# Performance work log

Hardware: AMD Instinct MI355X
Metric: run time of the kernel (lower is better)

The kernel has to match this reference:

```python
import math
import jax, jax.numpy as jnp
import numpy as np

B, S, C, H, W = 2, 4, 64, 256, 256
CI = 3 * C + 2      # per-sweep router input channels (Sz,Tz,delta + 2 pos)
CO = CI // 8        # compress_ratio = 8 -> 24
ENC = S * CO        # 96
HID = 64
TEMP = 0.7
ALPHA_ADV, BETA_BAND = 1.0, 0.5
BAND_L, BAND_H = 0.05, 0.2
W_HEUR, W_LEAR = 0.5, 0.5


def group_norm(x, gamma, beta, groups, eps=1e-5):
    b, c, h, w = x.shape
    xg = x.reshape(b, groups, c // groups, h, w)
    mu = xg.mean(axis=(2, 3, 4), keepdims=True)
    var = xg.var(axis=(2, 3, 4), keepdims=True)
    xg = (xg - mu) / jnp.sqrt(var + eps)
    return xg.reshape(b, c, h, w) * gamma[None, :, None, None] + beta[None, :, None, None]


def setup_inputs() -> dict:
    key = jax.random.key(0)
    ks = jax.random.split(key, 6)
    return {
        "S_feat": jax.random.normal(ks[0], (B, C, H, W), jnp.float32),
        "T_feat": jax.random.normal(ks[1], (B, S, C, H, W), jnp.float32),
        "adapter_w": jax.random.normal(ks[2], (S, C, C), jnp.float32) * 0.05,
        "adapter_b": jnp.zeros((S, C), jnp.float32),
        "ema_mu": jnp.zeros((1, S, C, 1, 1), jnp.float32),
        "ema_sigma": jnp.ones((1, S, C, 1, 1), jnp.float32),
        "ema_proxy": jnp.zeros((1, S, 1, 1, 1), jnp.float32),
        "enc_w": jax.random.normal(ks[3], (S, CO, CI), jnp.float32) * 0.05,
        "gn1_g": jnp.ones((ENC,), jnp.float32),
        "gn1_b": jnp.zeros((ENC,), jnp.float32),
        "mix1_w": jax.random.normal(ks[4], (HID, ENC), jnp.float32) * 0.05,
        "gn2_g": jnp.ones((HID,), jnp.float32),
        "gn2_b": jnp.zeros((HID,), jnp.float32),
        "mix2_w": jax.random.normal(ks[5], (S, HID), jnp.float32) * 0.05,
        "mix2_b": jnp.zeros((S,), jnp.float32),
    }


def reference(S_feat, T_feat, adapter_w, adapter_b, ema_mu, ema_sigma, ema_proxy,
              enc_w, gn1_g, gn1_b, mix1_w, gn2_g, gn2_b, mix2_w, mix2_b):
    # per-sweep 1x1 adapters applied to each teacher sweep and to the student feature
    bias = adapter_b[None, :, :, None, None]
    T_adapt = jnp.einsum('bsihw,soi->bsohw', T_feat, adapter_w) + bias   # [B,S,C,H,W]
    S_rep = jnp.einsum('bihw,soi->bsohw', S_feat, adapter_w) + bias      # [B,S,C,H,W]

    # EMA standardization (sigma clamped like clamp_min(1e-3))
    sigma = jnp.clip(ema_sigma, 1e-3, None)
    Tz = (T_adapt - ema_mu) / sigma
    Sz = (S_rep - ema_mu) / sigma
    delta = Sz - Tz

    # heuristic score: channel-mean squared discrepancy (advantage vs EMA proxy) + band bonus
    proxy = jnp.mean(delta ** 2, axis=2, keepdims=True)                  # [B,S,1,H,W]
    adv = proxy - ema_proxy
    band = ((proxy >= BAND_L) & (proxy <= BAND_H)).astype(proxy.dtype)
    heur = (ALPHA_ADV * adv + BETA_BAND * band)[:, :, 0]                 # [B,S,H,W]

    # sin positional embedding per sweep (pos_mode='sin', 2 channels)
    idx = jnp.linspace(0.0, 1.0, S)
    pos = jnp.stack([jnp.sin(2 * math.pi * idx), jnp.cos(2 * math.pi * idx)], axis=1)  # [S,2]
    pos = jnp.broadcast_to(pos[None, :, :, None, None], (Sz.shape[0], S, 2, Sz.shape[3], Sz.shape[4]))

    # learned router: grouped 1x1 encoder (groups=S) + GN/GELU mixer -> S spatial logits
    x = jnp.concatenate([Sz, Tz, delta, pos], axis=2)                    # [B,S,CI,H,W]
    enc = jnp.einsum('bsihw,soi->bsohw', x, enc_w)                       # grouped 1x1 conv
    enc = enc.reshape(enc.shape[0], ENC, enc.shape[3], enc.shape[4])
    h = jax.nn.gelu(group_norm(enc, gn1_g, gn1_b, 32), approximate=False)
    h = jnp.einsum('bchw,oc->bohw', h, mix1_w)
    h = jax.nn.gelu(group_norm(h, gn2_g, gn2_b, 32), approximate=False)
    lear = jnp.einsum('bchw,oc->bohw', h, mix2_w) + mix2_b[None, :, None, None]  # [B,S,H,W]

    # fuse heuristic + learned, temperature-scaled soft gating over sweeps
    logits = (W_HEUR * heur + W_LEAR * lear) / TEMP
    gates = jax.nn.softmax(logits, axis=1)[:, :, None]                   # [B,S,1,H,W]
    fused = jnp.sum(gates * T_adapt, axis=1)                             # [B,C,H,W]
    return fused
```

## Files before the change

### kernel.cpp

```cpp
#include <hip/hip_runtime.h>
#include <math.h>

#define B_   2
#define S_   4
#define C_   64
#define HW_  65536
#define CI_  194
#define CO_  24
#define ENC_ 96
#define HID_ 64
#define NSEG 8

__device__ __forceinline__ float gelu_f(float x){
  return 0.5f*x*(1.0f+erff(x*0.70710678118654752f));
}

__global__ void kPrep(const float* __restrict__ encw, float* __restrict__ E1,
                      float* __restrict__ E2, float* __restrict__ c0){
  int t = blockIdx.x*blockDim.x + threadIdx.x;
  int tot = S_*CO_*C_;
  for (int idx=t; idx<tot; idx += gridDim.x*blockDim.x){
    int c  = idx & (C_-1);
    int so = idx >> 6;
    const float* row = encw + so*CI_;
    E1[idx] = row[c]      + row[2*C_+c];
    E2[idx] = row[C_+c]   - row[2*C_+c];
  }
  if (t < S_*CO_){
    int s = t / CO_;
    float idxv = (float)s / 3.0f;
    float ang  = 6.283185307179586f * idxv;
    const float* row = encw + t*CI_;
    c0[t] = row[3*C_]*sinf(ang) + row[3*C_+1]*cosf(ang);
  }
}

__global__ __launch_bounds__(256, 4) void kAdapterEnc(
    const float* __restrict__ Sf, const float* __restrict__ Tf,
    const float* __restrict__ adW, const float* __restrict__ adB,
    const float* __restrict__ mu, const float* __restrict__ sg,
    const float* __restrict__ eproxy,
    const float* __restrict__ E1, const float* __restrict__ E2,
    const float* __restrict__ c0,
    float* __restrict__ enc, float* __restrict__ heur, float* __restrict__ Ta)
{
  const int hw = blockIdx.x*256 + threadIdx.x;
  const int b  = blockIdx.y;
  const int s  = blockIdx.z;

  __shared__ float w_sh[C_][C_];
  __shared__ float e_sh[C_][2*CO_];
  __shared__ float bias_sh[C_], mu_sh[C_], inv_sh[C_], c0_sh[CO_];

  for (int idx=threadIdx.x; idx<C_*C_; idx+=256){
    int oc=idx>>6, i=idx&63;
    w_sh[oc][i] = adW[(s*C_+oc)*C_+i];
  }
  for (int idx=threadIdx.x; idx<C_*CO_; idx+=256){
    int oc=idx/CO_, e=idx-oc*CO_;
    e_sh[oc][e]     = E1[(s*CO_+e)*C_+oc];
    e_sh[oc][CO_+e] = E2[(s*CO_+e)*C_+oc];
  }
  if (threadIdx.x<C_){
    bias_sh[threadIdx.x]=adB[s*C_+threadIdx.x];
    mu_sh[threadIdx.x]  =mu [s*C_+threadIdx.x];
    inv_sh[threadIdx.x] =1.0f/fmaxf(sg[s*C_+threadIdx.x],1e-3f);
  }
  if (threadIdx.x<CO_) c0_sh[threadIdx.x]=c0[s*CO_+threadIdx.x];
  __syncthreads();

  const float* tbase = Tf + ((size_t)(b*S_+s)*C_)*HW_ + hw;
  const float* sbase = Sf + ((size_t)b*C_)*HW_ + hw;
  float* tabase      = Ta + ((size_t)(b*S_+s)*C_)*HW_ + hw;

  float eacc[CO_];
#pragma unroll
  for (int e=0;e<CO_;e++) eacc[e]=c0_sh[e];
  float pacc=0.f;

  for (int oc0=0; oc0<C_; oc0+=16){
    float ta[16], sr[16];
#pragma unroll
    for (int k=0;k<16;k++){ ta[k]=bias_sh[oc0+k]; sr[k]=ta[k]; }

    for (int i0=0;i0<C_;i0+=8){
      float ti[8], si[8];
#pragma unroll
      for (int ii=0;ii<8;ii++){
        ti[ii]=tbase[(size_t)(i0+ii)*HW_];
        si[ii]=sbase[(size_t)(i0+ii)*HW_];
      }
#pragma unroll
      for (int k=0;k<16;k++){
        float4 w0=*(const float4*)&w_sh[oc0+k][i0];
        float4 w1=*(const float4*)&w_sh[oc0+k][i0+4];
        ta[k]=fmaf(w0.x,ti[0],ta[k]); sr[k]=fmaf(w0.x,si[0],sr[k]);
        ta[k]=fmaf(w0.y,ti[1],ta[k]); sr[k]=fmaf(w0.y,si[1],sr[k]);
        ta[k]=fmaf(w0.z,ti[2],ta[k]); sr[k]=fmaf(w0.z,si[2],sr[k]);
        ta[k]=fmaf(w0.w,ti[3],ta[k]); sr[k]=fmaf(w0.w,si[3],sr[k]);
        ta[k]=fmaf(w1.x,ti[4],ta[k]); sr[k]=fmaf(w1.x,si[4],sr[k]);
        ta[k]=fmaf(w1.y,ti[5],ta[k]); sr[k]=fmaf(w1.y,si[5],sr[k]);
        ta[k]=fmaf(w1.z,ti[6],ta[k]); sr[k]=fmaf(w1.z,si[6],sr[k]);
        ta[k]=fmaf(w1.w,ti[7],ta[k]); sr[k]=fmaf(w1.w,si[7],sr[k]);
      }
    }
#pragma unroll
    for (int k=0;k<16;k++){
      int oc=oc0+k;
      tabase[(size_t)oc*HW_] = ta[k];
      float m=mu_sh[oc], inv=inv_sh[oc];
      float tz=(ta[k]-m)*inv;
      float sz=(sr[k]-m)*inv;
      float d=sz-tz; pacc=fmaf(d,d,pacc);
#pragma unroll
      for (int e0=0;e0<CO_;e0+=4){
        float4 E1v=*(const float4*)&e_sh[oc][e0];
        float4 E2v=*(const float4*)&e_sh[oc][CO_+e0];
        eacc[e0+0]=fmaf(E1v.x,sz,fmaf(E2v.x,tz,eacc[e0+0]));
        eacc[e0+1]=fmaf(E1v.y,sz,fmaf(E2v.y,tz,eacc[e0+1]));
        eacc[e0+2]=fmaf(E1v.z,sz,fmaf(E2v.z,tz,eacc[e0+2]));
        eacc[e0+3]=fmaf(E1v.w,sz,fmaf(E2v.w,tz,eacc[e0+3]));
      }
    }
  }

  float proxy = pacc*(1.0f/(float)C_);
  float adv   = proxy - eproxy[s];
  float band  = (proxy>=0.05f && proxy<=0.2f)?1.0f:0.0f;
  heur[((size_t)(b*S_+s))*HW_+hw] = adv + 0.5f*band;
#pragma unroll
  for (int e=0;e<CO_;e++) enc[((size_t)((b*S_+s)*CO_+e))*HW_+hw] = eacc[e];
}

__global__ __launch_bounds__(256) void kStatsPart(const float* __restrict__ x, int npg, int nct,
  float* __restrict__ psum, float* __restrict__ psq)
{
  const int g=blockIdx.x, b=blockIdx.y, seg=blockIdx.z;
  const int F4_PER_SEG = HW_/4/NSEG;
  float sum=0.f, sq=0.f;
  for (int j=0;j<npg;j++){
    const float4* row=(const float4*)(x + (size_t)(b*nct+g*npg+j)*HW_) + seg*F4_PER_SEG;
    for (int i=threadIdx.x;i<F4_PER_SEG;i+=256){
      float4 v=row[i];
      sum += (v.x+v.y)+(v.z+v.w);
      sq = fmaf(v.x,v.x,sq); sq=fmaf(v.y,v.y,sq); sq=fmaf(v.z,v.z,sq); sq=fmaf(v.w,v.w,sq);
    }
  }
#pragma unroll
  for (int off=32;off>=1;off>>=1){ sum+=__shfl_xor(sum,off); sq+=__shfl_xor(sq,off); }
  __shared__ float ss[4], qq[4];
  int wid=threadIdx.x>>6, lane=threadIdx.x&63;
  if(lane==0){ ss[wid]=sum; qq[wid]=sq; }
  __syncthreads();
  if(threadIdx.x==0){
    psum[(b*32+g)*NSEG+seg]=ss[0]+ss[1]+ss[2]+ss[3];
    psq [(b*32+g)*NSEG+seg]=qq[0]+qq[1]+qq[2]+qq[3];
  }
}

__global__ void kFinalize(const float* __restrict__ psum, const float* __restrict__ psq,
  const float* __restrict__ gamma, const float* __restrict__ beta,
  int npg, int nct, float* __restrict__ cA, float* __restrict__ cB)
{
  int t=threadIdx.x;
  if (t < B_*32){
    int b=t>>5, g=t&31;
    float Ssum=0.f,Q=0.f;
    for(int k=0;k<NSEG;k++){ Ssum+=psum[t*NSEG+k]; Q+=psq[t*NSEG+k]; }
    float n=(float)npg*(float)HW_;
    float mean=Ssum/n;
    float var=Q/n-mean*mean;
    float inv=1.0f/sqrtf(var+1e-5f);
    for(int j=0;j<npg;j++){
      int c=g*npg+j;
      float a=gamma[c]*inv;
      cA[b*nct+c]=a;
      cB[b*nct+c]=beta[c]-mean*a;
    }
  }
}

__global__ __launch_bounds__(256, 4) void kMix1(
  const float* __restrict__ enc, const float* __restrict__ cA1, const float* __restrict__ cB1,
  const float* __restrict__ m1w, float* __restrict__ h1)
{
  const int hw=blockIdx.x*256+threadIdx.x;
  const int b=blockIdx.y;
  const int oh=blockIdx.z;

  __shared__ float w_sh[ENC_][32];
  __shared__ float a_sh[ENC_], c_sh[ENC_];
  for (int idx=threadIdx.x; idx<ENC_*32; idx+=256){
    int c=idx>>5, o=idx&31;
    w_sh[c][o]=m1w[(oh*32+o)*ENC_+c];
  }
  if (threadIdx.x<ENC_){
    a_sh[threadIdx.x]=cA1[b*ENC_+threadIdx.x];
    c_sh[threadIdx.x]=cB1[b*ENC_+threadIdx.x];
  }
  __syncthreads();

  float acc[32];
#pragma unroll
  for (int o=0;o<32;o++) acc[o]=0.f;

  for (int c0=0;c0<ENC_;c0+=8){
    float g8[8];
#pragma unroll
    for (int j=0;j<8;j++){
      float v=enc[((size_t)b*ENC_+c0+j)*HW_+hw];
      v=fmaf(v,a_sh[c0+j],c_sh[c0+j]);
      g8[j]=gelu_f(v);
    }
#pragma unroll
    for (int j=0;j<8;j++){
#pragma unroll
      for (int o4=0;o4<32;o4+=4){
        float4 w=*(const float4*)&w_sh[c0+j][o4];
        acc[o4+0]=fmaf(w.x,g8[j],acc[o4+0]);
        acc[o4+1]=fmaf(w.y,g8[j],acc[o4+1]);
        acc[o4+2]=fmaf(w.z,g8[j],acc[o4+2]);
        acc[o4+3]=fmaf(w.w,g8[j],acc[o4+3]);
      }
    }
  }
#pragma unroll
  for (int o=0;o<32;o++) h1[((size_t)(b*HID_+oh*32+o))*HW_+hw]=acc[o];
}

__global__ __launch_bounds__(256, 4) void kFinal(
  const float* __restrict__ Ta, const float* __restrict__ h1,
  const float* __restrict__ heur,
  const float* __restrict__ cA2, const float* __restrict__ cB2,
  const float* __restrict__ m2w, const float* __restrict__ m2b,
  float* __restrict__ out)
{
  const int hw = blockIdx.x*256+threadIdx.x;
  const int b  = blockIdx.y;
  const int ch = blockIdx.z;

  __shared__ float m2_sh[HID_][S_];
  __shared__ float a_sh[HID_], c_sh[HID_];
  __shared__ float m2b_sh[S_];

  for (int idx=threadIdx.x; idx<HID_*S_; idx+=256){
    int s=idx&3, c=idx>>2;
    m2_sh[c][s]=m2w[s*HID_+c];
  }
  if (threadIdx.x<HID_){
    a_sh[threadIdx.x]=cA2[b*HID_+threadIdx.x];
    c_sh[threadIdx.x]=cB2[b*HID_+threadIdx.x];
  }
  if (threadIdx.x<S_) m2b_sh[threadIdx.x]=m2b[threadIdx.x];
  __syncthreads();

  float la[S_];
#pragma unroll
  for (int s=0;s<S_;s++) la[s]=m2b_sh[s];
  for (int c0=0;c0<HID_;c0+=8){
#pragma unroll
    for (int j=0;j<8;j++){
      float v=h1[((size_t)b*HID_+c0+j)*HW_+hw];
      v=fmaf(v,a_sh[c0+j],c_sh[c0+j]);
      float g=gelu_f(v);
      float4 w=*(const float4*)&m2_sh[c0+j][0];
      la[0]=fmaf(w.x,g,la[0]); la[1]=fmaf(w.y,g,la[1]);
      la[2]=fmaf(w.z,g,la[2]); la[3]=fmaf(w.w,g,la[3]);
    }
  }
  float g0,g1,g2,g3;
  {
    float mx=-1e30f;
#pragma unroll
    for (int s=0;s<S_;s++){
      float hv=heur[((size_t)(b*S_+s))*HW_+hw];
      la[s]=(0.5f*hv+0.5f*la[s])*(1.0f/0.7f);
      mx=fmaxf(mx,la[s]);
    }
    float e0=expf(la[0]-mx), e1=expf(la[1]-mx), e2=expf(la[2]-mx), e3=expf(la[3]-mx);
    float dinv=1.0f/(e0+e1+e2+e3);
    g0=e0*dinv; g1=e1*dinv; g2=e2*dinv; g3=e3*dinv;
  }

  const float* ta0 = Ta + ((size_t)(b*S_+0)*C_ + ch*32)*HW_ + hw;
  const float* ta1 = ta0 + (size_t)C_*HW_;
  const float* ta2 = ta1 + (size_t)C_*HW_;
  const float* ta3 = ta2 + (size_t)C_*HW_;
  float* ob = out + ((size_t)(b*C_) + ch*32)*HW_ + hw;
#pragma unroll 8
  for (int k=0;k<32;k++){
    size_t o=(size_t)k*HW_;
    float v = g0*ta0[o];
    v = fmaf(g1, ta1[o], v);
    v = fmaf(g2, ta2[o], v);
    v = fmaf(g3, ta3[o], v);
    ob[o]=v;
  }
}

extern "C" void kernel_launch(void* const* d_in, const int* in_sizes, int n_in,
                              void* d_out, int out_size, void* d_ws, size_t ws_size,
                              hipStream_t stream) {
  (void)in_sizes; (void)n_in; (void)out_size; (void)ws_size;
  const float* Sf    = (const float*)d_in[0];
  const float* Tf    = (const float*)d_in[1];
  const float* adW   = (const float*)d_in[2];
  const float* adB   = (const float*)d_in[3];
  const float* mu    = (const float*)d_in[4];
  const float* sg    = (const float*)d_in[5];
  const float* eprox = (const float*)d_in[6];
  const float* encw  = (const float*)d_in[7];
  const float* gn1g  = (const float*)d_in[8];
  const float* gn1b  = (const float*)d_in[9];
  const float* m1w   = (const float*)d_in[10];
  const float* gn2g  = (const float*)d_in[11];
  const float* gn2b  = (const float*)d_in[12];
  const float* m2w   = (const float*)d_in[13];
  const float* m2b   = (const float*)d_in[14];
  float* out = (float*)d_out;

  float* ws = (float*)d_ws;
  size_t off = 0;
  float* Ta   = ws+off; off += (size_t)B_*S_*C_*HW_;
  float* enc  = ws+off; off += (size_t)B_*ENC_*HW_;
  float* h1   = ws+off; off += (size_t)B_*HID_*HW_;
  float* heur = ws+off; off += (size_t)B_*S_*HW_;
  float* E1   = ws+off; off += S_*CO_*C_;
  float* E2   = ws+off; off += S_*CO_*C_;
  float* c0   = ws+off; off += S_*CO_;
  float* ps1  = ws+off; off += B_*32*NSEG;
  float* pq1  = ws+off; off += B_*32*NSEG;
  float* ps2  = ws+off; off += B_*32*NSEG;
  float* pq2  = ws+off; off += B_*32*NSEG;
  float* cA1  = ws+off; off += B_*ENC_;
  float* cB1  = ws+off; off += B_*ENC_;
  float* cA2  = ws+off; off += B_*HID_;
  float* cB2  = ws+off; off += B_*HID_;

  kPrep<<<dim3(24), 256, 0, stream>>>(encw, E1, E2, c0);
  kAdapterEnc<<<dim3(HW_/256, B_, S_), 256, 0, stream>>>(Sf, Tf, adW, adB, mu, sg, eprox,
                                                         E1, E2, c0, enc, heur, Ta);
  kStatsPart<<<dim3(32, B_, NSEG), 256, 0, stream>>>(enc, 3, ENC_, ps1, pq1);
  kFinalize<<<1, 64, 0, stream>>>(ps1, pq1, gn1g, gn1b, 3, ENC_, cA1, cB1);
  kMix1<<<dim3(HW_/256, B_, 2), 256, 0, stream>>>(enc, cA1, cB1, m1w, h1);
  kStatsPart<<<dim3(32, B_, NSEG), 256, 0, stream>>>(h1, 2, HID_, ps2, pq2);
  kFinalize<<<1, 64, 0, stream>>>(ps2, pq2, gn2g, gn2b, 2, HID_, cA2, cB2);
  kFinal<<<dim3(HW_/256, B_, 2), 256, 0, stream>>>(Ta, h1, heur,
                                                   cA2, cB2, m2w, m2b, out);
}
```

Measured before the change: 733.7 us.

## Fuse GroupNorm statistics into producer kernels via atomics and read weights directly

Removes the two separate statistics passes over enc and h1. The producing kernels now reduce per-group sum and sum-of-squares across each block and atomically add them into global accumulators, which kPrep zeroes. It also drops the shared-memory staging of weights in all three big kernels. Weights are instead read straight from global memory with wave-uniform addresses, which frees LDS and lets the launch bounds ask for more waves. The risks are scalar-load and register pressure in the inner loops, float atomics that make the sums order-dependent, and the sum/sumsq variance formula being less precise.

```diff
diff --git a/kernel.cpp b/kernel.cpp
--- a/kernel.cpp
+++ b/kernel.cpp
@@ -9,22 +9,25 @@
 #define CO_  24
 #define ENC_ 96
 #define HID_ 64
-#define NSEG 8
 
 __device__ __forceinline__ float gelu_f(float x){
   return 0.5f*x*(1.0f+erff(x*0.70710678118654752f));
 }
 
-__global__ void kPrep(const float* __restrict__ encw, float* __restrict__ E1,
-                      float* __restrict__ E2, float* __restrict__ c0){
+__global__ void kPrep(const float* __restrict__ encw, float* __restrict__ E1t,
+                      float* __restrict__ E2t, float* __restrict__ c0,
+                      float* __restrict__ gs1, float* __restrict__ gq1,
+                      float* __restrict__ gs2, float* __restrict__ gq2){
   int t = blockIdx.x*blockDim.x + threadIdx.x;
-  int tot = S_*CO_*C_;
+  int tot = S_*C_*CO_;
   for (int idx=t; idx<tot; idx += gridDim.x*blockDim.x){
-    int c  = idx & (C_-1);
-    int so = idx >> 6;
-    const float* row = encw + so*CI_;
-    E1[idx] = row[c]      + row[2*C_+c];
-    E2[idx] = row[C_+c]   - row[2*C_+c];
+    int e   = idx % CO_;
+    int soc = idx / CO_;
+    int oc  = soc & (C_-1);
+    int s   = soc >> 6;
+    const float* row = encw + (s*CO_+e)*CI_;
+    E1t[idx] = row[oc]      + row[2*C_+oc];
+    E2t[idx] = row[C_+oc]   - row[2*C_+oc];
   }
   if (t < S_*CO_){
     int s = t / CO_;
@@ -33,55 +36,39 @@
     const float* row = encw + t*CI_;
     c0[t] = row[3*C_]*sinf(ang) + row[3*C_+1]*cosf(ang);
   }
-}
-
-__global__ __launch_bounds__(256, 4) void kAdapterEnc(
+  if (blockIdx.x==0 && threadIdx.x < B_*32){
+    gs1[threadIdx.x]=0.f; gq1[threadIdx.x]=0.f;
+    gs2[threadIdx.x]=0.f; gq2[threadIdx.x]=0.f;
+  }
+}
+
+__global__ __launch_bounds__(256, 5) void kAdapterEnc(
     const float* __restrict__ Sf, const float* __restrict__ Tf,
     const float* __restrict__ adW, const float* __restrict__ adB,
     const float* __restrict__ mu, const float* __restrict__ sg,
     const float* __restrict__ eproxy,
-    const float* __restrict__ E1, const float* __restrict__ E2,
+    const float* __restrict__ E1t, const float* __restrict__ E2t,
     const float* __restrict__ c0,
-    float* __restrict__ enc, float* __restrict__ heur, float* __restrict__ Ta)
+    float* __restrict__ enc, float* __restrict__ heur, float* __restrict__ Ta,
+    float* __restrict__ gs1, float* __restrict__ gq1)
 {
   const int hw = blockIdx.x*256 + threadIdx.x;
   const int b  = blockIdx.y;
   const int s  = blockIdx.z;
 
-  __shared__ float w_sh[C_][C_];
-  __shared__ float e_sh[C_][2*CO_];
-  __shared__ float bias_sh[C_], mu_sh[C_], inv_sh[C_], c0_sh[CO_];
-
-  for (int idx=threadIdx.x; idx<C_*C_; idx+=256){
-    int oc=idx>>6, i=idx&63;
-    w_sh[oc][i] = adW[(s*C_+oc)*C_+i];
-  }
-  for (int idx=threadIdx.x; idx<C_*CO_; idx+=256){
-    int oc=idx/CO_, e=idx-oc*CO_;
-    e_sh[oc][e]     = E1[(s*CO_+e)*C_+oc];
-    e_sh[oc][CO_+e] = E2[(s*CO_+e)*C_+oc];
-  }
-  if (threadIdx.x<C_){
-    bias_sh[threadIdx.x]=adB[s*C_+threadIdx.x];
-    mu_sh[threadIdx.x]  =mu [s*C_+threadIdx.x];
-    inv_sh[threadIdx.x] =1.0f/fmaxf(sg[s*C_+threadIdx.x],1e-3f);
-  }
-  if (threadIdx.x<CO_) c0_sh[threadIdx.x]=c0[s*CO_+threadIdx.x];
-  __syncthreads();
-
   const float* tbase = Tf + ((size_t)(b*S_+s)*C_)*HW_ + hw;
   const float* sbase = Sf + ((size_t)b*C_)*HW_ + hw;
   float* tabase      = Ta + ((size_t)(b*S_+s)*C_)*HW_ + hw;
 
   float eacc[CO_];
 #pragma unroll
-  for (int e=0;e<CO_;e++) eacc[e]=c0_sh[e];
+  for (int e=0;e<CO_;e++) eacc[e]=c0[s*CO_+e];
   float pacc=0.f;
 
   for (int oc0=0; oc0<C_; oc0+=16){
     float ta[16], sr[16];
 #pragma unroll
-    for (int k=0;k<16;k++){ ta[k]=bias_sh[oc0+k]; sr[k]=ta[k]; }
+    for (int k=0;k<16;k++){ float bb=adB[s*C_+oc0+k]; ta[k]=bb; sr[k]=bb; }
 
     for (int i0=0;i0<C_;i0+=8){
       float ti[8], si[8];
@@ -92,35 +79,30 @@
       }
 #pragma unroll
       for (int k=0;k<16;k++){
-        float4 w0=*(const float4*)&w_sh[oc0+k][i0];
-        float4 w1=*(const float4*)&w_sh[oc0+k][i0+4];
-        ta[k]=fmaf(w0.x,ti[0],ta[k]); sr[k]=fmaf(w0.x,si[0],sr[k]);
-        ta[k]=fmaf(w0.y,ti[1],ta[k]); sr[k]=fmaf(w0.y,si[1],sr[k]);
-        ta[k]=fmaf(w0.z,ti[2],ta[k]); sr[k]=fmaf(w0.z,si[2],sr[k]);
-        ta[k]=fmaf(w0.w,ti[3],ta[k]); sr[k]=fmaf(w0.w,si[3],sr[k]);
-        ta[k]=fmaf(w1.x,ti[4],ta[k]); sr[k]=fmaf(w1.x,si[4],sr[k]);
-        ta[k]=fmaf(w1.y,ti[5],ta[k]); sr[k]=fmaf(w1.y,si[5],sr[k]);
-        ta[k]=fmaf(w1.z,ti[6],ta[k]); sr[k]=fmaf(w1.z,si[6],sr[k]);
-        ta[k]=fmaf(w1.w,ti[7],ta[k]); sr[k]=fmaf(w1.w,si[7],sr[k]);
+        const float* wr = adW + (size_t)(s*C_+oc0+k)*C_ + i0;
+#pragma unroll
+        for (int ii=0;ii<8;ii++){
+          float w = wr[ii];
+          ta[k]=fmaf(w,ti[ii],ta[k]);
+          sr[k]=fmaf(w,si[ii],sr[k]);
+        }
       }
     }
 #pragma unroll
     for (int k=0;k<16;k++){
       int oc=oc0+k;
       tabase[(size_t)oc*HW_] = ta[k];
-      float m=mu_sh[oc], inv=inv_sh[oc];
+      float m   = mu[s*C_+oc];
+      float sig = fmaxf(sg[s*C_+oc],1e-3f);
+      float inv = 1.0f/sig;
       float tz=(ta[k]-m)*inv;
       float sz=(sr[k]-m)*inv;
       float d=sz-tz; pacc=fmaf(d,d,pacc);
-#pragma unroll
-      for (int e0=0;e0<CO_;e0+=4){
-        float4 E1v=*(const float4*)&e_sh[oc][e0];
-        float4 E2v=*(const float4*)&e_sh[oc][CO_+e0];
-        eacc[e0+0]=fmaf(E1v.x,sz,fmaf(E2v.x,tz,eacc[e0+0]));
-        eacc[e0+1]=fmaf(E1v.y,sz,fmaf(E2v.y,tz,eacc[e0+1]));
-        eacc[e0+2]=fmaf(E1v.z,sz,fmaf(E2v.z,tz,eacc[e0+2]));
-        eacc[e0+3]=fmaf(E1v.w,sz,fmaf(E2v.w,tz,eacc[e0+3]));
-      }
+      const float* e1 = E1t + (size_t)(s*C_+oc)*CO_;
+      const float* e2 = E2t + (size_t)(s*C_+oc)*CO_;
+#pragma unroll
+      for (int e=0;e<CO_;e++)
+        eacc[e]=fmaf(e1[e],sz,fmaf(e2[e],tz,eacc[e]));
     }
   }
 
@@ -130,43 +112,34 @@
   heur[((size_t)(b*S_+s))*HW_+hw] = adv + 0.5f*band;
 #pragma unroll
   for (int e=0;e<CO_;e++) enc[((size_t)((b*S_+s)*CO_+e))*HW_+hw] = eacc[e];
-}
-
-__global__ __launch_bounds__(256) void kStatsPart(const float* __restrict__ x, int npg, int nct,
-  float* __restrict__ psum, float* __restrict__ psq)
-{
-  const int g=blockIdx.x, b=blockIdx.y, seg=blockIdx.z;
-  const int F4_PER_SEG = HW_/4/NSEG;
-  float sum=0.f, sq=0.f;
-  for (int j=0;j<npg;j++){
-    const float4* row=(const float4*)(x + (size_t)(b*nct+g*npg+j)*HW_) + seg*F4_PER_SEG;
-    for (int i=threadIdx.x;i<F4_PER_SEG;i+=256){
-      float4 v=row[i];
-      sum += (v.x+v.y)+(v.z+v.w);
-      sq = fmaf(v.x,v.x,sq); sq=fmaf(v.y,v.y,sq); sq=fmaf(v.z,v.z,sq); sq=fmaf(v.w,v.w,sq);
-    }
-  }
-#pragma unroll
-  for (int off=32;off>=1;off>>=1){ sum+=__shfl_xor(sum,off); sq+=__shfl_xor(sq,off); }
-  __shared__ float ss[4], qq[4];
-  int wid=threadIdx.x>>6, lane=threadIdx.x&63;
-  if(lane==0){ ss[wid]=sum; qq[wid]=sq; }
+
+  __shared__ float red[2][4][8];
+  int lane=threadIdx.x&63, wid=threadIdx.x>>6;
+#pragma unroll
+  for (int j=0;j<8;j++){
+    float sm = eacc[3*j]+eacc[3*j+1]+eacc[3*j+2];
+    float sq = eacc[3*j]*eacc[3*j]+eacc[3*j+1]*eacc[3*j+1]+eacc[3*j+2]*eacc[3*j+2];
+#pragma unroll
+    for (int off=32;off>=1;off>>=1){ sm+=__shfl_xor(sm,off); sq+=__shfl_xor(sq,off); }
+    if (lane==0){ red[0][wid][j]=sm; red[1][wid][j]=sq; }
+  }
   __syncthreads();
-  if(threadIdx.x==0){
-    psum[(b*32+g)*NSEG+seg]=ss[0]+ss[1]+ss[2]+ss[3];
-    psq [(b*32+g)*NSEG+seg]=qq[0]+qq[1]+qq[2]+qq[3];
-  }
-}
-
-__global__ void kFinalize(const float* __restrict__ psum, const float* __restrict__ psq,
+  if (threadIdx.x<16){
+    int j=threadIdx.x&7, which=threadIdx.x>>3;
+    float v = red[which][0][j]+red[which][1][j]+red[which][2][j]+red[which][3][j];
+    float* dst = which ? gq1 : gs1;
+    atomicAdd(&dst[b*32 + 8*s + j], v);
+  }
+}
+
+__global__ void kFinalize(const float* __restrict__ gsum, const float* __restrict__ gsq,
   const float* __restrict__ gamma, const float* __restrict__ beta,
   int npg, int nct, float* __restrict__ cA, float* __restrict__ cB)
 {
   int t=threadIdx.x;
   if (t < B_*32){
     int b=t>>5, g=t&31;
-    float Ssum=0.f,Q=0.f;
-    for(int k=0;k<NSEG;k++){ Ssum+=psum[t*NSEG+k]; Q+=psq[t*NSEG+k]; }
+    float Ssum=gsum[t], Q=gsq[t];
     float n=(float)npg*(float)HW_;
     float mean=Ssum/n;
     float var=Q/n-mean*mean;
@@ -180,26 +153,15 @@
   }
 }
 
-__global__ __launch_bounds__(256, 4) void kMix1(
+__global__ __launch_bounds__(256, 6) void kMix1(
   const float* __restrict__ enc, const float* __restrict__ cA1, const float* __restrict__ cB1,
-  const float* __restrict__ m1w, float* __restrict__ h1)
+  const float* __restrict__ m1w, float* __restrict__ h1,
+  float* __restrict__ gs2, float* __restrict__ gq2)
 {
   const int hw=blockIdx.x*256+threadIdx.x;
   const int b=blockIdx.y;
   const int oh=blockIdx.z;
 
-  __shared__ float w_sh[ENC_][32];
-  __shared__ float a_sh[ENC_], c_sh[ENC_];
-  for (int idx=threadIdx.x; idx<ENC_*32; idx+=256){
-    int c=idx>>5, o=idx&31;
-    w_sh[c][o]=m1w[(oh*32+o)*ENC_+c];
-  }
-  if (threadIdx.x<ENC_){
-    a_sh[threadIdx.x]=cA1[b*ENC_+threadIdx.x];
-    c_sh[threadIdx.x]=cB1[b*ENC_+threadIdx.x];
-  }
-  __syncthreads();
-
   float acc[32];
 #pragma unroll
   for (int o=0;o<32;o++) acc[o]=0.f;
@@ -209,23 +171,40 @@
 #pragma unroll
     for (int j=0;j<8;j++){
       float v=enc[((size_t)b*ENC_+c0+j)*HW_+hw];
-      v=fmaf(v,a_sh[c0+j],c_sh[c0+j]);
+      v=fmaf(v,cA1[b*ENC_+c0+j],cB1[b*ENC_+c0+j]);
       g8[j]=gelu_f(v);
     }
 #pragma unroll
-    for (int j=0;j<8;j++){
-#pragma unroll
-      for (int o4=0;o4<32;o4+=4){
-        float4 w=*(const float4*)&w_sh[c0+j][o4];
-        acc[o4+0]=fmaf(w.x,g8[j],acc[o4+0]);
-        acc[o4+1]=fmaf(w.y,g8[j],acc[o4+1]);
-        acc[o4+2]=fmaf(w.z,g8[j],acc[o4+2]);
-        acc[o4+3]=fmaf(w.w,g8[j],acc[o4+3]);
-      }
+    for (int o=0;o<32;o++){
+      const float* wr = m1w + (size_t)(oh*32+o)*ENC_ + c0;
+      float a=acc[o];
+      a=fmaf(wr[0],g8[0],a); a=fmaf(wr[1],g8[1],a);
+      a=fmaf(wr[2],g8[2],a); a=fmaf(wr[3],g8[3],a);
+      a=fmaf(wr[4],g8[4],a); a=fmaf(wr[5],g8[5],a);
+      a=fmaf(wr[6],g8[6],a); a=fmaf(wr[7],g8[7],a);
+      acc[o]=a;
     }
   }
 #pragma unroll
   for (int o=0;o<32;o++) h1[((size_t)(b*HID_+oh*32+o))*HW_+hw]=acc[o];
+
+  __shared__ float red[2][4][16];
+  int lane=threadIdx.x&63, wid=threadIdx.x>>6;
+#pragma unroll
+  for (int j=0;j<16;j++){
+    float sm = acc[2*j]+acc[2*j+1];
+    float sq = acc[2*j]*acc[2*j]+acc[2*j+1]*acc[2*j+1];
+#pragma unroll
+    for (int off=32;off>=1;off>>=1){ sm+=__shfl_xor(sm,off); sq+=__shfl_xor(sq,off); }
+    if (lane==0){ red[0][wid][j]=sm; red[1][wid][j]=sq; }
+  }
+  __syncthreads();
+  if (threadIdx.x<32){
+    int j=threadIdx.x&15, which=threadIdx.x>>4;
+    float v = red[which][0][j]+red[which][1][j]+red[which][2][j]+red[which][3][j];
+    float* dst = which ? gq2 : gs2;
+    atomicAdd(&dst[b*32 + oh*16 + j], v);
+  }
 }
 
 __global__ __launch_bounds__(256, 4) void kFinal(
@@ -239,33 +218,20 @@
   const int b  = blockIdx.y;
   const int ch = blockIdx.z;
 
-  __shared__ float m2_sh[HID_][S_];
-  __shared__ float a_sh[HID_], c_sh[HID_];
-  __shared__ float m2b_sh[S_];
-
-  for (int idx=threadIdx.x; idx<HID_*S_; idx+=256){
-    int s=idx&3, c=idx>>2;
-    m2_sh[c][s]=m2w[s*HID_+c];
-  }
-  if (threadIdx.x<HID_){
-    a_sh[threadIdx.x]=cA2[b*HID_+threadIdx.x];
-    c_sh[threadIdx.x]=cB2[b*HID_+threadIdx.x];
-  }
-  if (threadIdx.x<S_) m2b_sh[threadIdx.x]=m2b[threadIdx.x];
-  __syncthreads();
-
   float la[S_];
 #pragma unroll
-  for (int s=0;s<S_;s++) la[s]=m2b_sh[s];
+  for (int s=0;s<S_;s++) la[s]=m2b[s];
   for (int c0=0;c0<HID_;c0+=8){
 #pragma unroll
     for (int j=0;j<8;j++){
-      float v=h1[((size_t)b*HID_+c0+j)*HW_+hw];
-      v=fmaf(v,a_sh[c0+j],c_sh[c0+j]);
+      int c=c0+j;
+      float v=h1[((size_t)b*HID_+c)*HW_+hw];
+      v=fmaf(v,cA2[b*HID_+c],cB2[b*HID_+c]);
       float g=gelu_f(v);
-      float4 w=*(const float4*)&m2_sh[c0+j][0];
-      la[0]=fmaf(w.x,g,la[0]); la[1]=fmaf(w.y,g,la[1]);
-      la[2]=fmaf(w.z,g,la[2]); la[3]=fmaf(w.w,g,la[3]);
+      la[0]=fmaf(m2w[0*HID_+c],g,la[0]);
+      la[1]=fmaf(m2w[1*HID_+c],g,la[1]);
+      la[2]=fmaf(m2w[2*HID_+c],g,la[2]);
+      la[3]=fmaf(m2w[3*HID_+c],g,la[3]);
     }
   }
   float g0,g1,g2,g3;
@@ -325,26 +291,25 @@
   float* enc  = ws+off; off += (size_t)B_*ENC_*HW_;
   float* h1   = ws+off; off += (size_t)B_*HID_*HW_;
   float* heur = ws+off; off += (size_t)B_*S_*HW_;
-  float* E1   = ws+off; off += S_*CO_*C_;
-  float* E2   = ws+off; off += S_*CO_*C_;
+  float* E1t  = ws+off; off += S_*C_*CO_;
+  float* E2t  = ws+off; off += S_*C_*CO_;
   float* c0   = ws+off; off += S_*CO_;
-  float* ps1  = ws+off; off += B_*32*NSEG;
-  float* pq1  = ws+off; off += B_*32*NSEG;
-  float* ps2  = ws+off; off += B_*32*NSEG;
-  float* pq2  = ws+off; off += B_*32*NSEG;
+  float* gs1  = ws+off; off += B_*32;
+  float* gq1  = ws+off; off += B_*32;
+  float* gs2  = ws+off; off += B_*32;
+  float* gq2  = ws+off; off += B_*32;
   float* cA1  = ws+off; off += B_*ENC_;
   float* cB1  = ws+off; off += B_*ENC_;
   float* cA2  = ws+off; off += B_*HID_;
   float* cB2  = ws+off; off += B_*HID_;
 
-  kPrep<<<dim3(24), 256, 0, stream>>>(encw, E1, E2, c0);
+  kPrep<<<dim3(24), 256, 0, stream>>>(encw, E1t, E2t, c0, gs1, gq1, gs2, gq2);
   kAdapterEnc<<<dim3(HW_/256, B_, S_), 256, 0, stream>>>(Sf, Tf, adW, adB, mu, sg, eprox,
-                                                         E1, E2, c0, enc, heur, Ta);
-  kStatsPart<<<dim3(32, B_, NSEG), 256, 0, stream>>>(enc, 3, ENC_, ps1, pq1);
-  kFinalize<<<1, 64, 0, stream>>>(ps1, pq1, gn1g, gn1b, 3, ENC_, cA1, cB1);
-  kMix1<<<dim3(HW_/256, B_, 2), 256, 0, stream>>>(enc, cA1, cB1, m1w, h1);
-  kStatsPart<<<dim3(32, B_, NSEG), 256, 0, stream>>>(h1, 2, HID_, ps2, pq2);
-  kFinalize<<<1, 64, 0, stream>>>(ps2, pq2, gn2g, gn2b, 2, HID_, cA2, cB2);
+                                                         E1t, E2t, c0, enc, heur, Ta,
+                                                         gs1, gq1);
+  kFinalize<<<1, 64, 0, stream>>>(gs1, gq1, gn1g, gn1b, 3, ENC_, cA1, cB1);
+  kMix1<<<dim3(HW_/256, B_, 2), 256, 0, stream>>>(enc, cA1, cB1, m1w, h1, gs2, gq2);
+  kFinalize<<<1, 64, 0, stream>>>(gs2, gq2, gn2g, gn2b, 2, HID_, cA2, cB2);
   kFinal<<<dim3(HW_/256, B_, 2), 256, 0, stream>>>(Ta, h1, heur,
                                                    cA2, cB2, m2w, m2b, out);
 }
```

Result: faster. 628.3 us (-14.4%).
